# Kernel optimization log

Hardware: AMD Instinct MI355X
Metric: run time of the kernel (lower is better)

The kernel has to match this reference:

```python
import jax, jax.numpy as jnp
import numpy as np

N_PTS = 100000
C_IN, C_OUT, K = 16, 32, 3
B, D, H, W = 2, 32, 128, 128


def setup_inputs() -> dict:
    key = jax.random.key(0)
    kf, kw, kb, kz, ky, kx = jax.random.split(key, 6)
    features = jax.random.normal(kf, (N_PTS, C_IN), dtype=jnp.float32)
    coords = jnp.stack([
        jax.random.randint(kb, (N_PTS,), 0, B),
        jax.random.randint(kz, (N_PTS,), 0, D),
        jax.random.randint(ky, (N_PTS,), 0, H),
        jax.random.randint(kx, (N_PTS,), 0, W),
    ], axis=1).astype(jnp.int32)
    weight = jax.random.normal(kw, (K ** 3, C_IN, C_OUT), dtype=jnp.float32) * 0.01
    bias = jnp.zeros((C_OUT,), dtype=jnp.float32)
    return {"features": features, "coords": coords, "weight": weight, "bias": bias,
            "batch_size": B, "d_sp": D, "h_sp": H, "w_sp": W}


def reference(features, coords, weight, bias, batch_size, d_sp, h_sp, w_sp):
    # Scatter sparse voxel features into dense grid (B, C_in, D, H, W).
    n, c_in = features.shape
    c_out = weight.shape[2]
    k = K
    b, z, y, x = coords[:, 0], coords[:, 1], coords[:, 2], coords[:, 3]
    dense = jnp.zeros((batch_size, c_in, d_sp, h_sp, w_sp), dtype=features.dtype)
    dense = dense.at[b, :, z, y, x].set(features)  # (N,) advanced idx -> rows of (N, C_in)
    # Conv3d: torch copies weight.view(C_out, C_in, k, k, k) -> OIDHW kernel.
    kernel = weight.reshape(c_out, c_in, k, k, k)
    out = jax.lax.conv_general_dilated(
        dense, kernel,
        window_strides=(1, 1, 1),
        padding=[(1, 1), (1, 1), (1, 1)],
        dimension_numbers=("NCDHW", "OIDHW", "NCDHW"))
    out = jax.nn.relu(out + bias[None, :, None, None, None])
    # Dense equivalent of the torch nonzero-gather (which has data-dependent
    # shape): return the full dense activated grid (B, C_out, D, H, W).
    return out
```

## Files before the change

### kernel.cpp

```cpp
#include <hip/hip_runtime.h>

#define CIN   16
#define COUT  32
#define BATCH 2
#define DSP   32
#define HSP   128
#define WSP   128
#define NVOX  (BATCH*DSP*HSP*WSP)

#define DP (DSP+2)
#define HP (HSP+2)
#define WP (WSP+2)
#define NVOXP (BATCH*DP*HP*WP)
#define NDCH  (NVOXP*2)

#define TZ 2
#define TY 8
#define TX 16
#define NTW 8
#define PZ 4
#define PYY 10
#define PXX 18
#define PROW (PYY*PXX)
#define PVOX (PZ*PROW)
#define NCHUNK (2*PVOX)
#define SLICE  (NCHUNK/8)
#define NPAIR 14
#define NWEL  (NPAIR*2*64*8)
#define NWREP ((NWEL + 255)/256)
#define NBLK  512

typedef __bf16 bf16x8 __attribute__((ext_vector_type(8)));
typedef float  f32x4  __attribute__((ext_vector_type(4)));

__device__ __forceinline__ void load_lds16(const void* g, void* l) {
    __builtin_amdgcn_global_load_lds(
        (const __attribute__((address_space(1))) unsigned*)g,
        (__attribute__((address_space(3))) unsigned*)l, 16, 0, 0);
}

__global__ void k_prep(const int4* __restrict__ coords, int n, int nbDedup,
                       int* __restrict__ map,
                       const float* __restrict__ w, __bf16* __restrict__ wpack) {
    int bb = blockIdx.x;
    if (bb < nbDedup) {
        int p = bb * 256 + threadIdx.x;
        if (p >= n) return;
        int4 c = coords[p];
        int vox = ((c.x*DSP + c.y)*HSP + c.z)*WSP + c.w;
        atomicMax(&map[vox], p);
    } else {
        int i = (bb - nbDedup) * 256 + threadIdx.x;
        if (i >= NWEL) return;
        int j = i & 7, l = (i>>3) & 63, h = (i>>9) & 1, p = i >> 10;
        int tap = 2*p + ((l>>4)>>1);
        int co  = h*16 + (l & 15);
        int ci  = ((l>>4)&1)*8 + j;
        float v = (tap < 27) ? w[(co*CIN + ci)*27 + tap] : 0.0f;
        wpack[i] = (__bf16)v;
    }
}

__global__ void k_fill(const int* __restrict__ map, const float* __restrict__ feat,
                       __bf16* __restrict__ dense) {
    int c = blockIdx.x * 256 + threadIdx.x;
    if (c >= NDCH) return;
    int v = c >> 1, h = c & 1;
    int bb = v / (DP*HP*WP);
    int r  = v - bb*(DP*HP*WP);
    int zp = r / (HP*WP);  r -= zp*(HP*WP);
    int yp = r / WP;
    int xp = r - yp*WP;
    bf16x8 val = { (__bf16)0.f,(__bf16)0.f,(__bf16)0.f,(__bf16)0.f,
                   (__bf16)0.f,(__bf16)0.f,(__bf16)0.f,(__bf16)0.f };
    if ((unsigned)(zp-1) < DSP && (unsigned)(yp-1) < HSP && (unsigned)(xp-1) < WSP) {
        int vox = ((bb*DSP + (zp-1))*HSP + (yp-1))*WSP + (xp-1);
        int p = map[vox];
        if (p >= 0) {
            const float4* fp = (const float4*)(feat + (size_t)p*CIN) + h*2;
            float4 f0 = fp[0], f1 = fp[1];
            val = bf16x8{ (__bf16)f0.x,(__bf16)f0.y,(__bf16)f0.z,(__bf16)f0.w,
                          (__bf16)f1.x,(__bf16)f1.y,(__bf16)f1.z,(__bf16)f1.w };
        }
    }
    *(bf16x8*)(dense + (size_t)v*CIN + h*8) = val;
}

__device__ __forceinline__ void stage_tile(const __bf16* __restrict__ gb,
                                           ushort* lbase, int wave, int lane) {
    #pragma unroll
    for (int it = 0; it < 3; ++it) {
        int rel = it*64 + lane;
        if (rel < SLICE) {
            int j = wave*SLICE + rel;
            int h = (j >= PVOX) ? 1 : 0;
            int v = j - h*PVOX;
            int pz = v / PROW;
            int rm = v - pz*PROW;
            int py = rm / PXX;
            int px = rm - py*PXX;
            load_lds16(gb + ((size_t)(pz*HP*WP + py*WP + px))*CIN + h*8,
                       (void*)(lbase + (size_t)(wave*SLICE + it*64)*8));
        }
    }
}

__global__ __launch_bounds__(512, 4) void k_conv(
    const __bf16* __restrict__ dense, const __bf16* __restrict__ wpack,
    const float* __restrict__ bias, float* __restrict__ out)
{
    __shared__ __align__(16) ushort patch[3][NCHUNK*8];

    int bid = blockIdx.x;
    int bs  = (bid & 7) * (NBLK/8) + (bid >> 3);
    int tyi = bs & 15, tzi = (bs >> 4) & 15, b = bs >> 8;
    int z0 = tzi*TZ, y0 = tyi*TY;

    int tid  = threadIdx.x;
    int lane = tid & 63, wave = tid >> 6;
    int lx16  = lane & 15;
    int lhalf = (lane >> 4) & 1;
    int ltp   = (lane >> 4) >> 1;
    int lq    = lane >> 4;
    int zw    = wave >> 2;
    int ysub  = (wave & 3) * 2;

    int voff[NPAIR];
    #pragma unroll
    for (int p = 0; p < NPAIR; ++p) {
        int tap = 2*p + ltp; if (tap > 26) tap = 26;
        int kd = tap/9, kh = (tap/3)%3, kw = tap%3;
        voff[p] = (kd*PYY + kh)*PXX + kw;
    }
    float bv0 = bias[lx16], bv1 = bias[16 + lx16];
    const __bf16* wl = wpack + (size_t)lane*8;

    const __bf16* gbase = dense + ((((size_t)b*DP + z0)*HP + y0)*WP)*CIN;

    stage_tile(gbase, patch[0], wave, lane);

    int cur = 0;
    #pragma unroll 1
    for (int t = 0; t < NTW; ++t) {
        if (t == 0) asm volatile("s_waitcnt vmcnt(0)\ns_barrier"  ::: "memory");
        else        asm volatile("s_waitcnt vmcnt(32)\ns_barrier" ::: "memory");
        __builtin_amdgcn_sched_barrier(0);

        int nxt = (cur == 2) ? 0 : cur + 1;
        if (t < NTW-1)
            stage_tile(gbase + (size_t)(t+1)*TX*CIN, patch[nxt], wave, lane);
        __builtin_amdgcn_sched_barrier(0);

        f32x4 acc[2][2];
        acc[0][0] = (f32x4){0.f,0.f,0.f,0.f}; acc[0][1] = (f32x4){0.f,0.f,0.f,0.f};
        acc[1][0] = (f32x4){0.f,0.f,0.f,0.f}; acc[1][1] = (f32x4){0.f,0.f,0.f,0.f};
        const ushort* pb = patch[cur] +
            ((size_t)lhalf*PVOX + (zw*PYY + ysub)*PXX + lx16)*8;
        __builtin_amdgcn_s_setprio(1);
        #pragma unroll
        for (int p = 0; p < NPAIR; ++p) {
            bf16x8 w0 = *(const bf16x8*)(wl + (size_t)(p*2+0)*512);
            bf16x8 w1 = *(const bf16x8*)(wl + (size_t)(p*2+1)*512);
            const ushort* pa = pb + (size_t)voff[p]*8;
            #pragma unroll
            for (int gi = 0; gi < 2; ++gi) {
                bf16x8 a = *(const bf16x8*)(pa + gi*(PXX*8));
                acc[gi][0] = __builtin_amdgcn_mfma_f32_16x16x32_bf16(a, w0, acc[gi][0], 0,0,0);
                acc[gi][1] = __builtin_amdgcn_mfma_f32_16x16x32_bf16(a, w1, acc[gi][1], 0,0,0);
            }
        }
        __builtin_amdgcn_s_setprio(0);

        #pragma unroll
        for (int gi = 0; gi < 2; ++gi) {
            int gz = z0 + zw, gy = y0 + ysub + gi;
            int gx = t*TX + (lq << 2);
            f32x4 o0, o1;
            o0[0] = fmaxf(acc[gi][0][0]+bv0, 0.f); o0[1] = fmaxf(acc[gi][0][1]+bv0, 0.f);
            o0[2] = fmaxf(acc[gi][0][2]+bv0, 0.f); o0[3] = fmaxf(acc[gi][0][3]+bv0, 0.f);
            o1[0] = fmaxf(acc[gi][1][0]+bv1, 0.f); o1[1] = fmaxf(acc[gi][1][1]+bv1, 0.f);
            o1[2] = fmaxf(acc[gi][1][2]+bv1, 0.f); o1[3] = fmaxf(acc[gi][1][3]+bv1, 0.f);
            size_t base0 = ((((size_t)b*COUT + lx16)*DSP + gz)*HSP + gy)*WSP + gx;
            size_t base1 = base0 + (size_t)16*DSP*HSP*WSP;
            *(f32x4*)(out + base0) = o0;
            *(f32x4*)(out + base1) = o1;
        }
        cur = nxt;
    }
}

extern "C" void kernel_launch(void* const* d_in, const int* in_sizes, int n_in,
                              void* d_out, int out_size, void* d_ws, size_t ws_size,
                              hipStream_t stream) {
    const float* feat   = (const float*)d_in[0];
    const int4*  coords = (const int4*)d_in[1];
    const float* weight = (const float*)d_in[2];
    const float* bias   = (const float*)d_in[3];
    float* out = (float*)d_out;
    int n = in_sizes[0] / CIN;

    int*    map   = (int*)d_ws;
    __bf16* dense = (__bf16*)(map + NVOX);
    __bf16* wpack = dense + (size_t)NVOXP*CIN;

    (void)hipMemsetAsync(map, 0xFF, (size_t)NVOX*sizeof(int), stream);

    int nb = (n + 255) / 256;
    k_prep<<<nb + NWREP, 256, 0, stream>>>(coords, n, nb, map, weight, wpack);
    k_fill<<<(NDCH + 255)/256, 256, 0, stream>>>(map, feat, dense);
    k_conv<<<NBLK, 512, 0, stream>>>(dense, wpack, bias, out);
}
```

Before: 85.11 us.

## Shrink conv blocks to 4 waves, hold weights in registers, double-buffer LDS

The conv kernel now uses 256-thread blocks, each covering half as many y rows, and launches twice as many blocks. All weight fragments are loaded once into registers per thread, so the inner loop no longer issues global weight loads. The LDS patch ring goes from triple to double buffering: the next tile is staged first, then the kernel waits on vmcnt and adds an extra barrier after the MFMA loop. Register pressure rises sharply from about 112 VGPRs of weights, and the smaller y tile means more halo rows are re-fetched per output.

```diff
diff --git a/kernel.cpp b/kernel.cpp
--- a/kernel.cpp
+++ b/kernel.cpp
@@ -15,20 +15,20 @@
 #define NDCH  (NVOXP*2)
 
 #define TZ 2
-#define TY 8
+#define TY 4
 #define TX 16
 #define NTW 8
 #define PZ 4
-#define PYY 10
+#define PYY 6
 #define PXX 18
 #define PROW (PYY*PXX)
 #define PVOX (PZ*PROW)
 #define NCHUNK (2*PVOX)
-#define SLICE  (NCHUNK/8)
+#define SLICE  (NCHUNK/4)
 #define NPAIR 14
 #define NWEL  (NPAIR*2*64*8)
 #define NWREP ((NWEL + 255)/256)
-#define NBLK  512
+#define NBLK  1024
 
 typedef __bf16 bf16x8 __attribute__((ext_vector_type(8)));
 typedef float  f32x4  __attribute__((ext_vector_type(4)));
@@ -89,7 +89,7 @@
 __device__ __forceinline__ void stage_tile(const __bf16* __restrict__ gb,
                                            ushort* lbase, int wave, int lane) {
     #pragma unroll
-    for (int it = 0; it < 3; ++it) {
+    for (int it = 0; it < 4; ++it) {
         int rel = it*64 + lane;
         if (rel < SLICE) {
             int j = wave*SLICE + rel;
@@ -105,15 +105,15 @@
     }
 }
 
-__global__ __launch_bounds__(512, 4) void k_conv(
+__global__ __launch_bounds__(256, 3) void k_conv(
     const __bf16* __restrict__ dense, const __bf16* __restrict__ wpack,
     const float* __restrict__ bias, float* __restrict__ out)
 {
-    __shared__ __align__(16) ushort patch[3][NCHUNK*8];
+    __shared__ __align__(16) ushort patch[2][NCHUNK*8];
 
     int bid = blockIdx.x;
     int bs  = (bid & 7) * (NBLK/8) + (bid >> 3);
-    int tyi = bs & 15, tzi = (bs >> 4) & 15, b = bs >> 8;
+    int tyi = bs & 31, tzi = (bs >> 5) & 15, b = bs >> 9;
     int z0 = tzi*TZ, y0 = tyi*TY;
 
     int tid  = threadIdx.x;
@@ -122,8 +122,15 @@
     int lhalf = (lane >> 4) & 1;
     int ltp   = (lane >> 4) >> 1;
     int lq    = lane >> 4;
-    int zw    = wave >> 2;
-    int ysub  = (wave & 3) * 2;
+    int zw    = wave >> 1;
+    int yb    = (wave & 1) * 2;
+
+    bf16x8 wf[NPAIR][2];
+    #pragma unroll
+    for (int p = 0; p < NPAIR; ++p)
+        #pragma unroll
+        for (int h = 0; h < 2; ++h)
+            wf[p][h] = *(const bf16x8*)(wpack + (size_t)((p*2 + h)*64 + lane)*8);
 
     int voff[NPAIR];
     #pragma unroll
@@ -133,47 +140,45 @@
         voff[p] = (kd*PYY + kh)*PXX + kw;
     }
     float bv0 = bias[lx16], bv1 = bias[16 + lx16];
-    const __bf16* wl = wpack + (size_t)lane*8;
 
     const __bf16* gbase = dense + ((((size_t)b*DP + z0)*HP + y0)*WP)*CIN;
 
     stage_tile(gbase, patch[0], wave, lane);
 
-    int cur = 0;
     #pragma unroll 1
     for (int t = 0; t < NTW; ++t) {
-        if (t == 0) asm volatile("s_waitcnt vmcnt(0)\ns_barrier"  ::: "memory");
-        else        asm volatile("s_waitcnt vmcnt(32)\ns_barrier" ::: "memory");
-        __builtin_amdgcn_sched_barrier(0);
-
-        int nxt = (cur == 2) ? 0 : cur + 1;
         if (t < NTW-1)
-            stage_tile(gbase + (size_t)(t+1)*TX*CIN, patch[nxt], wave, lane);
+            stage_tile(gbase + (size_t)(t+1)*TX*CIN, patch[(t&1)^1], wave, lane);
+        if (t == 0 || t == NTW-1)
+            asm volatile("s_waitcnt vmcnt(4)\ns_barrier" ::: "memory");
+        else
+            asm volatile("s_waitcnt vmcnt(8)\ns_barrier" ::: "memory");
         __builtin_amdgcn_sched_barrier(0);
 
         f32x4 acc[2][2];
         acc[0][0] = (f32x4){0.f,0.f,0.f,0.f}; acc[0][1] = (f32x4){0.f,0.f,0.f,0.f};
         acc[1][0] = (f32x4){0.f,0.f,0.f,0.f}; acc[1][1] = (f32x4){0.f,0.f,0.f,0.f};
-        const ushort* pb = patch[cur] +
-            ((size_t)lhalf*PVOX + (zw*PYY + ysub)*PXX + lx16)*8;
+        const ushort* pb = patch[t&1] +
+            ((size_t)lhalf*PVOX + (zw*PYY + yb)*PXX + lx16)*8;
         __builtin_amdgcn_s_setprio(1);
         #pragma unroll
         for (int p = 0; p < NPAIR; ++p) {
-            bf16x8 w0 = *(const bf16x8*)(wl + (size_t)(p*2+0)*512);
-            bf16x8 w1 = *(const bf16x8*)(wl + (size_t)(p*2+1)*512);
             const ushort* pa = pb + (size_t)voff[p]*8;
             #pragma unroll
             for (int gi = 0; gi < 2; ++gi) {
                 bf16x8 a = *(const bf16x8*)(pa + gi*(PXX*8));
-                acc[gi][0] = __builtin_amdgcn_mfma_f32_16x16x32_bf16(a, w0, acc[gi][0], 0,0,0);
-                acc[gi][1] = __builtin_amdgcn_mfma_f32_16x16x32_bf16(a, w1, acc[gi][1], 0,0,0);
+                acc[gi][0] = __builtin_amdgcn_mfma_f32_16x16x32_bf16(a, wf[p][0], acc[gi][0], 0,0,0);
+                acc[gi][1] = __builtin_amdgcn_mfma_f32_16x16x32_bf16(a, wf[p][1], acc[gi][1], 0,0,0);
             }
         }
         __builtin_amdgcn_s_setprio(0);
+
+        asm volatile("s_barrier" ::: "memory");
+        __builtin_amdgcn_sched_barrier(0);
 
         #pragma unroll
         for (int gi = 0; gi < 2; ++gi) {
-            int gz = z0 + zw, gy = y0 + ysub + gi;
+            int gz = z0 + zw, gy = y0 + yb + gi;
             int gx = t*TX + (lq << 2);
             f32x4 o0, o1;
             o0[0] = fmaxf(acc[gi][0][0]+bv0, 0.f); o0[1] = fmaxf(acc[gi][0][1]+bv0, 0.f);
@@ -185,7 +190,6 @@
             *(f32x4*)(out + base0) = o0;
             *(f32x4*)(out + base1) = o1;
         }
-        cur = nxt;
     }
 }
 
@@ -208,5 +212,5 @@
     int nb = (n + 255) / 256;
     k_prep<<<nb + NWREP, 256, 0, stream>>>(coords, n, nb, map, weight, wpack);
     k_fill<<<(NDCH + 255)/256, 256, 0, stream>>>(map, feat, dense);
-    k_conv<<<NBLK, 512, 0, stream>>>(dense, wpack, bias, out);
-}
+    k_conv<<<NBLK, 256, 0, stream>>>(dense, wpack, bias, out);
+}
```

Result: faster. 69.54 us (-18.3%).
